# Kernel optimization log

Measured on AMD Instinct MI355X. Metric: run time of the kernel, lower is better.

Reference implementation:

```python
import jax, jax.numpy as jnp
import numpy as np

N, F, H, C, E = 100000, 128, 128, 32, 600000


def setup_inputs() -> dict:
    key = jax.random.key(0)
    ks = jax.random.split(key, 8)
    x = jax.random.normal(ks[0], (N, F), dtype=jnp.float32)
    edge_index = jax.random.randint(ks[1], (2, E), 0, N, dtype=jnp.int64)
    s = 1.0 / np.sqrt(F)
    sh = 1.0 / np.sqrt(H)
    W1l = jax.random.uniform(ks[2], (F, H), jnp.float32, -s, s)
    W1r = jax.random.uniform(ks[3], (F, H), jnp.float32, -s, s)
    b1 = jnp.zeros((H,), jnp.float32)
    W2l = jax.random.uniform(ks[4], (H, C), jnp.float32, -sh, sh)
    W2r = jax.random.uniform(ks[5], (H, C), jnp.float32, -sh, sh)
    b2 = jnp.zeros((C,), jnp.float32)
    return {"x": x, "edge_index": edge_index, "W1l": W1l, "b1": b1,
            "W1r": W1r, "W2l": W2l, "b2": b2, "W2r": W2r}


def reference(x, edge_index, W1l, b1, W1r, W2l, b2, W2r):
    # PyG SAGEConv: out = lin_l(mean_{j in N(i)} x_j) + lin_r(x_i)
    # (lin_l has bias, lin_r does not). Dropout is identity in eval mode.
    src, dst = edge_index[0], edge_index[1]
    n = x.shape[0]
    deg = jax.ops.segment_sum(jnp.ones((src.shape[0],), x.dtype), dst, num_segments=n)
    inv_deg = 1.0 / jnp.maximum(deg, 1.0)  # clamp: isolated nodes get 0 agg

    def sage(h, Wl, bl, Wr):
        agg = jax.ops.segment_sum(h[src], dst, num_segments=n)  # [N, d] gather+scatter
        agg = agg * inv_deg[:, None]
        return agg @ Wl + bl + h @ Wr

    h = jax.nn.relu(sage(x, W1l, b1, W1r))
    return sage(h, W2l, b2, W2r)
```

## Files before the change

### kernel.cpp

```cpp
#include <hip/hip_runtime.h>
#include <hip/hip_bf16.h>


#define FDIM 128
#define CDIM 32
#define SCAN_CHUNK 1024
#define PSTR 136

typedef __attribute__((ext_vector_type(8))) short short8;
typedef __attribute__((ext_vector_type(4))) float f32x4;
typedef unsigned short ushort_t;
typedef unsigned int uint_t;

static __device__ __forceinline__ ushort_t f2bf(float f) {
    uint_t u = __float_as_uint(f);
    u += 0x7fffu + ((u >> 16) & 1u);
    return (ushort_t)(u >> 16);
}
static __device__ __forceinline__ float bf2f_lo(uint_t u) {
    return __uint_as_float(u << 16);
}
static __device__ __forceinline__ float bf2f_hi(uint_t u) {
    return __uint_as_float(u & 0xffff0000u);
}


__global__ __launch_bounds__(256) void prep_kernel(
        const float* __restrict__ x, uint_t* __restrict__ xb4, long long total8,
        const int* __restrict__ dst, int* __restrict__ deg, int E, int n,
        const float* __restrict__ W1l, const float* __restrict__ W1r,
        const float* __restrict__ W2l, const float* __restrict__ W2r,
        ushort_t* __restrict__ w1lt, ushort_t* __restrict__ w1rt,
        ushort_t* __restrict__ w2lt, ushort_t* __restrict__ w2rt,
        int CB, int DB) {
    int b = (int)blockIdx.x;
    if (b < CB) {
        long long i = (long long)b * 256 + threadIdx.x;
        if (i >= total8) return;
        const float4* p = (const float4*)x + i * 2;
        float4 v0 = p[0], v1 = p[1];
        uint4 o;
        o.x = (uint_t)f2bf(v0.x) | ((uint_t)f2bf(v0.y) << 16);
        o.y = (uint_t)f2bf(v0.z) | ((uint_t)f2bf(v0.w) << 16);
        o.z = (uint_t)f2bf(v1.x) | ((uint_t)f2bf(v1.y) << 16);
        o.w = (uint_t)f2bf(v1.z) | ((uint_t)f2bf(v1.w) << 16);
        ((uint4*)xb4)[i] = o;
    } else if (b < CB + DB) {
        int e = (b - CB) * 256 + threadIdx.x;
        if (e < E) {
            int d = dst[e];
            if (d >= 0 && d < n) atomicAdd(&deg[d], 1);
        }
    } else {
        int idx = (b - CB - DB) * 256 + threadIdx.x;
        const float* w; ushort_t* wt; int Nc, local;
        if (idx < 16384)      { w = W1l; wt = w1lt; Nc = 128; local = idx; }
        else if (idx < 32768) { w = W1r; wt = w1rt; Nc = 128; local = idx - 16384; }
        else if (idx < 36864) { w = W2l; wt = w2lt; Nc = 32;  local = idx - 32768; }
        else if (idx < 40960) { w = W2r; wt = w2rt; Nc = 32;  local = idx - 36864; }
        else return;
        int nn = local >> 7, kk = local & 127;
        wt[nn * 128 + kk] = f2bf(w[kk * Nc + nn]);
    }
}


__global__ __launch_bounds__(256) void scan1_kernel(
        const int* __restrict__ deg, int* __restrict__ partials, int n) {
    __shared__ int red[256];
    int t = threadIdx.x;
    int base = blockIdx.x * SCAN_CHUNK + t * 4;
    int s = 0;
    if (base + 3 < n) {
        int4 v = *(const int4*)(deg + base);
        s = v.x + v.y + v.z + v.w;
    } else {
        for (int i = 0; i < 4; i++) if (base + i < n) s += deg[base + i];
    }
    red[t] = s;
    __syncthreads();
#pragma unroll
    for (int off = 128; off > 0; off >>= 1) {
        if (t < off) red[t] += red[t + off];
        __syncthreads();
    }
    if (t == 0) partials[blockIdx.x] = red[0];
}

__global__ __launch_bounds__(256) void scan3_kernel(
        const int* __restrict__ deg, const int* __restrict__ partials,
        int* __restrict__ rowptr, float* __restrict__ inv_deg, int n, int SB) {
    __shared__ int s[256];
    int t = threadIdx.x;
    int pre = (t < SB && t < (int)blockIdx.x) ? partials[t] : 0;
    s[t] = pre;
    __syncthreads();
#pragma unroll
    for (int off = 128; off > 0; off >>= 1) {
        if (t < off) s[t] += s[t + off];
        __syncthreads();
    }
    int blockbase = s[0];
    __syncthreads();

    int base = blockIdx.x * SCAN_CHUNK + t * 4;
    int d0 = 0, d1 = 0, d2 = 0, d3 = 0;
    if (base + 3 < n) {
        int4 v = *(const int4*)(deg + base);
        d0 = v.x; d1 = v.y; d2 = v.z; d3 = v.w;
    } else {
        if (base + 0 < n) d0 = deg[base + 0];
        if (base + 1 < n) d1 = deg[base + 1];
        if (base + 2 < n) d2 = deg[base + 2];
        if (base + 3 < n) d3 = deg[base + 3];
    }
    s[t] = d0 + d1 + d2 + d3;
    __syncthreads();
#pragma unroll
    for (int off = 1; off < 256; off <<= 1) {
        int u = (t >= off) ? s[t - off] : 0;
        __syncthreads();
        s[t] += u;
        __syncthreads();
    }
    int run = blockbase + ((t == 0) ? 0 : s[t - 1]);
    int dd[4] = {d0, d1, d2, d3};
#pragma unroll
    for (int i = 0; i < 4; i++) {
        if (base + i < n) {
            rowptr[base + i]  = run;
            inv_deg[base + i] = 1.0f / (float)(dd[i] > 0 ? dd[i] : 1);
            run += dd[i];
        }
    }
}

__global__ void fill_kernel(const int* __restrict__ src, const int* __restrict__ dst,
                            const int* __restrict__ rowptr, int* __restrict__ cursor,
                            int* __restrict__ nbr, int E, int n) {
    int e = blockIdx.x * 256 + threadIdx.x;
    if (e < E) {
        int s = src[e];
        int d = dst[e];
        if (d >= 0 && d < n) {
            int p = atomicAdd(&cursor[d], 1);
            nbr[rowptr[d] + p] = s;
        }
    }
}


__global__ __launch_bounds__(256) void agg1_kernel(
        const uint_t* __restrict__ xbu ,
        const int* __restrict__ rowptr, const int* __restrict__ deg,
        const int* __restrict__ nbr, const float* __restrict__ inv_deg,
        uint_t* __restrict__ aggbu, int n) {
    int t = threadIdx.x;
    int i = blockIdx.x * 4 + (t >> 6);
    if (i >= n) return;
    int lane = t & 63;
    int g    = lane >> 4;
    int l16  = lane & 15;
    int start = rowptr[i];
    int d     = deg[i];
    float s[8] = {0.f, 0.f, 0.f, 0.f, 0.f, 0.f, 0.f, 0.f};
    int e = g;
    for (; e + 4 < d; e += 8) {
        int j0 = nbr[start + e];
        int j1 = nbr[start + e + 4];
        uint4 u0 = *(const uint4*)(xbu + (size_t)j0 * 64 + l16 * 4);
        uint4 u1 = *(const uint4*)(xbu + (size_t)j1 * 64 + l16 * 4);
        s[0] += bf2f_lo(u0.x) + bf2f_lo(u1.x); s[1] += bf2f_hi(u0.x) + bf2f_hi(u1.x);
        s[2] += bf2f_lo(u0.y) + bf2f_lo(u1.y); s[3] += bf2f_hi(u0.y) + bf2f_hi(u1.y);
        s[4] += bf2f_lo(u0.z) + bf2f_lo(u1.z); s[5] += bf2f_hi(u0.z) + bf2f_hi(u1.z);
        s[6] += bf2f_lo(u0.w) + bf2f_lo(u1.w); s[7] += bf2f_hi(u0.w) + bf2f_hi(u1.w);
    }
    if (e < d) {
        int j = nbr[start + e];
        uint4 u = *(const uint4*)(xbu + (size_t)j * 64 + l16 * 4);
        s[0] += bf2f_lo(u.x); s[1] += bf2f_hi(u.x);
        s[2] += bf2f_lo(u.y); s[3] += bf2f_hi(u.y);
        s[4] += bf2f_lo(u.z); s[5] += bf2f_hi(u.z);
        s[6] += bf2f_lo(u.w); s[7] += bf2f_hi(u.w);
    }
#pragma unroll
    for (int k = 0; k < 8; k++) {
        s[k] += __shfl_xor(s[k], 16, 64);
        s[k] += __shfl_xor(s[k], 32, 64);
    }
    if (g == 0) {
        float inv = inv_deg[i];
        uint4 o;
        o.x = (uint_t)f2bf(s[0] * inv) | ((uint_t)f2bf(s[1] * inv) << 16);
        o.y = (uint_t)f2bf(s[2] * inv) | ((uint_t)f2bf(s[3] * inv) << 16);
        o.z = (uint_t)f2bf(s[4] * inv) | ((uint_t)f2bf(s[5] * inv) << 16);
        o.w = (uint_t)f2bf(s[6] * inv) | ((uint_t)f2bf(s[7] * inv) << 16);
        *(uint4*)(aggbu + (size_t)i * 64 + l16 * 4) = o;
    }
}


__global__ __launch_bounds__(512) void fused12_kernel(
        const ushort_t* __restrict__ xb, const ushort_t* __restrict__ aggb,
        const ushort_t* __restrict__ w1lt, const ushort_t* __restrict__ w1rt,
        const ushort_t* __restrict__ w2lt, const ushort_t* __restrict__ w2rt,
        const float* __restrict__ b1,
        ushort_t* __restrict__ z2b, float* __restrict__ r2, int n) {
    __shared__ ushort_t xs[64 * PSTR];
    __shared__ ushort_t as_[64 * PSTR];
    __shared__ ushort_t ws2[2 * 32 * PSTR];

    const int t    = threadIdx.x;
    const int wave = t >> 6;
    const int lane = t & 63;
    const int quad = lane >> 4;
    const int l16  = lane & 15;
    const int row0 = blockIdx.x * 64;
    const int c1   = wave * 16;

#pragma unroll
    for (int it = 0; it < 2; it++) {
        int c   = t + it * 512;
        int row = c >> 4, col = c & 15;
        int grow = row0 + row; if (grow >= n) grow = n - 1;
        size_t goff = (size_t)grow * FDIM + col * 8;
        short8 vx = *(const short8*)(xb + goff);
        short8 va = *(const short8*)(aggb + goff);
        *(short8*)(xs  + row * PSTR + col * 8) = vx;
        *(short8*)(as_ + row * PSTR + col * 8) = va;
    }
#pragma unroll
    for (int it = 0; it < 2; it++) {
        int c = t + it * 512;
        int m = c >> 9, lo = c & 511;
        int row = lo >> 4, col = lo & 15;
        const ushort_t* sw = m ? w2rt : w2lt;
        *(short8*)(ws2 + (m * 32 + row) * PSTR + col * 8) =
            *(const short8*)(sw + row * 128 + col * 8);
    }

    short8 bl1[4], br1[4];
#pragma unroll
    for (int k = 0; k < 4; k++) {
        size_t woff = (size_t)(c1 + l16) * FDIM + k * 32 + quad * 8;
        bl1[k] = *(const short8*)(w1lt + woff);
        br1[k] = *(const short8*)(w1rt + woff);
    }
    float b1c = b1[c1 + l16];

    __syncthreads();

    f32x4 acc1[4];
#pragma unroll
    for (int r = 0; r < 4; r++) acc1[r] = (f32x4){0.f, 0.f, 0.f, 0.f};

#pragma unroll
    for (int k = 0; k < 4; k++) {
        short8 a1[4], a2[4];
#pragma unroll
        for (int r = 0; r < 4; r++) {
            int lro = (r * 16 + l16) * PSTR + k * 32 + quad * 8;
            a1[r] = *(const short8*)(as_ + lro);
            a2[r] = *(const short8*)(xs  + lro);
        }
#pragma unroll
        for (int r = 0; r < 4; r++) {
            acc1[r] = __builtin_amdgcn_mfma_f32_16x16x32_bf16(a1[r], bl1[k], acc1[r], 0, 0, 0);
            acc1[r] = __builtin_amdgcn_mfma_f32_16x16x32_bf16(a2[r], br1[k], acc1[r], 0, 0, 0);
        }
    }

    __syncthreads();

    ushort_t* hs = xs;
#pragma unroll
    for (int r = 0; r < 4; r++)
#pragma unroll
        for (int reg = 0; reg < 4; reg++) {
            int lrow = r * 16 + quad * 4 + reg;
            float v = acc1[r][reg] + b1c;
            v = v > 0.f ? v : 0.f;
            hs[lrow * PSTR + c1 + l16] = f2bf(v);
        }

    __syncthreads();

    const int rs = (wave >> 1) * 16;
    const int c2 = (wave & 1) * 16;
    f32x4 a2l = (f32x4){0.f, 0.f, 0.f, 0.f};
    f32x4 a2r = (f32x4){0.f, 0.f, 0.f, 0.f};
#pragma unroll
    for (int k = 0; k < 4; k++) {
        short8 ah = *(const short8*)(hs  + (rs + l16) * PSTR + k * 32 + quad * 8);
        short8 wl = *(const short8*)(ws2 + (c2 + l16) * PSTR + k * 32 + quad * 8);
        short8 wr = *(const short8*)(ws2 + (32 + c2 + l16) * PSTR + k * 32 + quad * 8);
        a2l = __builtin_amdgcn_mfma_f32_16x16x32_bf16(ah, wl, a2l, 0, 0, 0);
        a2r = __builtin_amdgcn_mfma_f32_16x16x32_bf16(ah, wr, a2r, 0, 0, 0);
    }
#pragma unroll
    for (int reg = 0; reg < 4; reg++) {
        int grow = row0 + rs + quad * 4 + reg;
        if (grow < n) {
            z2b[(size_t)grow * CDIM + c2 + l16] = f2bf(a2l[reg]);
            r2 [(size_t)grow * CDIM + c2 + l16] = a2r[reg];
        }
    }
}


__global__ __launch_bounds__(256) void combine2_kernel(
        const uint_t* __restrict__ z2bu ,
        const int* __restrict__ rowptr, const int* __restrict__ deg,
        const int* __restrict__ nbr, const float* __restrict__ inv_deg,
        const float* __restrict__ b2, const float* __restrict__ r2,
        float* __restrict__ out, int n) {
    int t = threadIdx.x;
    int i = blockIdx.x * 4 + (t >> 6);
    if (i >= n) return;
    int lane = t & 63;
    int g    = lane >> 4;
    int l16  = lane & 15;
    int start = rowptr[i];
    int d     = deg[i];
    float s0 = 0.f, s1 = 0.f;
    int e = g;
    for (; e + 4 < d; e += 8) {
        int j0 = nbr[start + e];
        int j1 = nbr[start + e + 4];
        uint_t u0 = z2bu[(size_t)j0 * 16 + l16];
        uint_t u1 = z2bu[(size_t)j1 * 16 + l16];
        s0 += bf2f_lo(u0) + bf2f_lo(u1);
        s1 += bf2f_hi(u0) + bf2f_hi(u1);
    }
    if (e < d) {
        int j = nbr[start + e];
        uint_t u = z2bu[(size_t)j * 16 + l16];
        s0 += bf2f_lo(u);
        s1 += bf2f_hi(u);
    }
    s0 += __shfl_xor(s0, 16, 64); s0 += __shfl_xor(s0, 32, 64);
    s1 += __shfl_xor(s1, 16, 64); s1 += __shfl_xor(s1, 32, 64);
    if (g == 0) {
        float inv = inv_deg[i];
        float2 rr = *(const float2*)(r2 + (size_t)i * CDIM + l16 * 2);
        float2 o;
        o.x = s0 * inv + rr.x + b2[l16 * 2];
        o.y = s1 * inv + rr.y + b2[l16 * 2 + 1];
        *(float2*)(out + (size_t)i * CDIM + l16 * 2) = o;
    }
}


extern "C" void kernel_launch(void* const* d_in, const int* in_sizes, int n_in,
                              void* d_out, int out_size, void* d_ws, size_t ws_size,
                              hipStream_t stream) {
    const float* x   = (const float*)d_in[0];
    const int*   ei  = (const int*)d_in[1];
    const float* W1l = (const float*)d_in[2];
    const float* b1  = (const float*)d_in[3];
    const float* W1r = (const float*)d_in[4];
    const float* W2l = (const float*)d_in[5];
    const float* b2  = (const float*)d_in[6];
    const float* W2r = (const float*)d_in[7];

    const int N = in_sizes[0] / FDIM;
    const int E = in_sizes[1] / 2;
    const int* src = ei;
    const int* dst = ei + E;

    char* p = (char*)d_ws;
    int*      deg      = (int*)p;      p += (size_t)N * sizeof(int);
    int*      cursor   = (int*)p;      p += (size_t)N * sizeof(int);
    int*      rowptr   = (int*)p;      p += (size_t)N * sizeof(int);
    float*    inv_deg  = (float*)p;    p += (size_t)N * sizeof(float);
    int*      partials = (int*)p;      p += 256 * sizeof(int);
    ushort_t* w1lt     = (ushort_t*)p; p += FDIM * FDIM * sizeof(ushort_t);
    ushort_t* w1rt     = (ushort_t*)p; p += FDIM * FDIM * sizeof(ushort_t);
    ushort_t* w2lt     = (ushort_t*)p; p += FDIM * CDIM * sizeof(ushort_t);
    ushort_t* w2rt     = (ushort_t*)p; p += FDIM * CDIM * sizeof(ushort_t);
    int*      nbr      = (int*)p;      p += (size_t)((E + 3) / 4 * 4) * sizeof(int);
    ushort_t* xb       = (ushort_t*)p; p += (size_t)N * FDIM * sizeof(ushort_t);
    ushort_t* aggb     = (ushort_t*)p; p += (size_t)N * FDIM * sizeof(ushort_t);
    ushort_t* z2b      = (ushort_t*)p; p += (size_t)N * CDIM * sizeof(ushort_t);
    float*    r2       = (float*)p;    p += (size_t)N * CDIM * sizeof(float);

    const int SB = (N + SCAN_CHUNK - 1) / SCAN_CHUNK;
    const long long total8 = (long long)N * FDIM / 8;
    const int CB = (int)((total8 + 255) / 256);
    const int DB = (E + 255) / 256;
    const int WB = (40960 + 255) / 256;

    hipMemsetAsync(deg, 0, 2 * (size_t)N * sizeof(int), stream);

    prep_kernel <<<CB + DB + WB, 256, 0, stream>>>(x, (uint_t*)xb, total8, dst, deg, E, N,
                                                   W1l, W1r, W2l, W2r,
                                                   w1lt, w1rt, w2lt, w2rt, CB, DB);
    scan1_kernel<<<SB, 256, 0, stream>>>(deg, partials, N);
    scan3_kernel<<<SB, 256, 0, stream>>>(deg, partials, rowptr, inv_deg, N, SB);
    fill_kernel <<<DB, 256, 0, stream>>>(src, dst, rowptr, cursor, nbr, E, N);

    agg1_kernel   <<<(N + 3) / 4, 256, 0, stream>>>((const uint_t*)xb, rowptr, deg, nbr,
                                                    inv_deg, (uint_t*)aggb, N);
    fused12_kernel<<<(N + 63) / 64, 512, 0, stream>>>(xb, aggb, w1lt, w1rt, w2lt, w2rt,
                                                      b1, z2b, r2, N);
    combine2_kernel<<<(N + 3) / 4, 256, 0, stream>>>((const uint_t*)z2b, rowptr, deg, nbr,
                                                     inv_deg, b2, r2, (float*)d_out, N);
}
```

Measured before the change: 255.8 us.

## Fuse layer-1 neighbor aggregation into the fused GEMM kernel via shared memory

Moves the layer-1 mean aggregation into fused12_kernel. Each wave gathers 8 rows' neighbor features and writes the bf16 mean straight into shared memory instead of into a global aggb buffer, which removes a 25.6 MB write and re-read plus one launch. Weight B-fragments are now loaded per k-step rather than held in registers, and launch bounds request higher occupancy. Degree counting is also split out of prep_kernel into its own kernel, so the latency-bound gather now sits inside a 512-thread block that also needs sync and LDS, which may cost occupancy and overlap.

```diff
diff --git a/kernel.cpp b/kernel.cpp
--- a/kernel.cpp
+++ b/kernel.cpp
@@ -25,14 +25,23 @@
 }
 
 
+__global__ void deg_kernel(const int* __restrict__ dst, int* __restrict__ deg,
+                           int E, int n) {
+    int e = blockIdx.x * 256 + threadIdx.x;
+    if (e < E) {
+        int d = dst[e];
+        if (d >= 0 && d < n) atomicAdd(&deg[d], 1);
+    }
+}
+
+
 __global__ __launch_bounds__(256) void prep_kernel(
         const float* __restrict__ x, uint_t* __restrict__ xb4, long long total8,
-        const int* __restrict__ dst, int* __restrict__ deg, int E, int n,
         const float* __restrict__ W1l, const float* __restrict__ W1r,
         const float* __restrict__ W2l, const float* __restrict__ W2r,
         ushort_t* __restrict__ w1lt, ushort_t* __restrict__ w1rt,
         ushort_t* __restrict__ w2lt, ushort_t* __restrict__ w2rt,
-        int CB, int DB) {
+        int CB) {
     int b = (int)blockIdx.x;
     if (b < CB) {
         long long i = (long long)b * 256 + threadIdx.x;
@@ -45,14 +54,8 @@
         o.z = (uint_t)f2bf(v1.x) | ((uint_t)f2bf(v1.y) << 16);
         o.w = (uint_t)f2bf(v1.z) | ((uint_t)f2bf(v1.w) << 16);
         ((uint4*)xb4)[i] = o;
-    } else if (b < CB + DB) {
-        int e = (b - CB) * 256 + threadIdx.x;
-        if (e < E) {
-            int d = dst[e];
-            if (d >= 0 && d < n) atomicAdd(&deg[d], 1);
-        }
     } else {
-        int idx = (b - CB - DB) * 256 + threadIdx.x;
+        int idx = (b - CB) * 256 + threadIdx.x;
         const float* w; ushort_t* wt; int Nc, local;
         if (idx < 16384)      { w = W1l; wt = w1lt; Nc = 128; local = idx; }
         else if (idx < 32768) { w = W1r; wt = w1rt; Nc = 128; local = idx - 16384; }
@@ -150,60 +153,12 @@
 }
 
 
-__global__ __launch_bounds__(256) void agg1_kernel(
-        const uint_t* __restrict__ xbu ,
+__global__ __launch_bounds__(512, 6) void fused12_kernel(
+        const ushort_t* __restrict__ xb, const uint_t* __restrict__ xbu,
+        const ushort_t* __restrict__ w1lt, const ushort_t* __restrict__ w1rt,
+        const ushort_t* __restrict__ w2lt, const ushort_t* __restrict__ w2rt,
         const int* __restrict__ rowptr, const int* __restrict__ deg,
         const int* __restrict__ nbr, const float* __restrict__ inv_deg,
-        uint_t* __restrict__ aggbu, int n) {
-    int t = threadIdx.x;
-    int i = blockIdx.x * 4 + (t >> 6);
-    if (i >= n) return;
-    int lane = t & 63;
-    int g    = lane >> 4;
-    int l16  = lane & 15;
-    int start = rowptr[i];
-    int d     = deg[i];
-    float s[8] = {0.f, 0.f, 0.f, 0.f, 0.f, 0.f, 0.f, 0.f};
-    int e = g;
-    for (; e + 4 < d; e += 8) {
-        int j0 = nbr[start + e];
-        int j1 = nbr[start + e + 4];
-        uint4 u0 = *(const uint4*)(xbu + (size_t)j0 * 64 + l16 * 4);
-        uint4 u1 = *(const uint4*)(xbu + (size_t)j1 * 64 + l16 * 4);
-        s[0] += bf2f_lo(u0.x) + bf2f_lo(u1.x); s[1] += bf2f_hi(u0.x) + bf2f_hi(u1.x);
-        s[2] += bf2f_lo(u0.y) + bf2f_lo(u1.y); s[3] += bf2f_hi(u0.y) + bf2f_hi(u1.y);
-        s[4] += bf2f_lo(u0.z) + bf2f_lo(u1.z); s[5] += bf2f_hi(u0.z) + bf2f_hi(u1.z);
-        s[6] += bf2f_lo(u0.w) + bf2f_lo(u1.w); s[7] += bf2f_hi(u0.w) + bf2f_hi(u1.w);
-    }
-    if (e < d) {
-        int j = nbr[start + e];
-        uint4 u = *(const uint4*)(xbu + (size_t)j * 64 + l16 * 4);
-        s[0] += bf2f_lo(u.x); s[1] += bf2f_hi(u.x);
-        s[2] += bf2f_lo(u.y); s[3] += bf2f_hi(u.y);
-        s[4] += bf2f_lo(u.z); s[5] += bf2f_hi(u.z);
-        s[6] += bf2f_lo(u.w); s[7] += bf2f_hi(u.w);
-    }
-#pragma unroll
-    for (int k = 0; k < 8; k++) {
-        s[k] += __shfl_xor(s[k], 16, 64);
-        s[k] += __shfl_xor(s[k], 32, 64);
-    }
-    if (g == 0) {
-        float inv = inv_deg[i];
-        uint4 o;
-        o.x = (uint_t)f2bf(s[0] * inv) | ((uint_t)f2bf(s[1] * inv) << 16);
-        o.y = (uint_t)f2bf(s[2] * inv) | ((uint_t)f2bf(s[3] * inv) << 16);
-        o.z = (uint_t)f2bf(s[4] * inv) | ((uint_t)f2bf(s[5] * inv) << 16);
-        o.w = (uint_t)f2bf(s[6] * inv) | ((uint_t)f2bf(s[7] * inv) << 16);
-        *(uint4*)(aggbu + (size_t)i * 64 + l16 * 4) = o;
-    }
-}
-
-
-__global__ __launch_bounds__(512) void fused12_kernel(
-        const ushort_t* __restrict__ xb, const ushort_t* __restrict__ aggb,
-        const ushort_t* __restrict__ w1lt, const ushort_t* __restrict__ w1rt,
-        const ushort_t* __restrict__ w2lt, const ushort_t* __restrict__ w2rt,
         const float* __restrict__ b1,
         ushort_t* __restrict__ z2b, float* __restrict__ r2, int n) {
     __shared__ ushort_t xs[64 * PSTR];
@@ -223,11 +178,8 @@
         int c   = t + it * 512;
         int row = c >> 4, col = c & 15;
         int grow = row0 + row; if (grow >= n) grow = n - 1;
-        size_t goff = (size_t)grow * FDIM + col * 8;
-        short8 vx = *(const short8*)(xb + goff);
-        short8 va = *(const short8*)(aggb + goff);
-        *(short8*)(xs  + row * PSTR + col * 8) = vx;
-        *(short8*)(as_ + row * PSTR + col * 8) = va;
+        short8 vx = *(const short8*)(xb + (size_t)grow * FDIM + col * 8);
+        *(short8*)(xs + row * PSTR + col * 8) = vx;
     }
 #pragma unroll
     for (int it = 0; it < 2; it++) {
@@ -239,23 +191,60 @@
             *(const short8*)(sw + row * 128 + col * 8);
     }
 
-    short8 bl1[4], br1[4];
+    for (int q = 0; q < 8; q++) {
+        int lrow = wave * 8 + q;
+        int i = row0 + lrow;
+        if (i >= n) break;
+        int start = rowptr[i];
+        int d     = deg[i];
+        float s[8] = {0.f, 0.f, 0.f, 0.f, 0.f, 0.f, 0.f, 0.f};
+        int e = quad;
+        for (; e + 4 < d; e += 8) {
+            int j0 = nbr[start + e];
+            int j1 = nbr[start + e + 4];
+            uint4 u0 = *(const uint4*)(xbu + (size_t)j0 * 64 + l16 * 4);
+            uint4 u1 = *(const uint4*)(xbu + (size_t)j1 * 64 + l16 * 4);
+            s[0] += bf2f_lo(u0.x) + bf2f_lo(u1.x); s[1] += bf2f_hi(u0.x) + bf2f_hi(u1.x);
+            s[2] += bf2f_lo(u0.y) + bf2f_lo(u1.y); s[3] += bf2f_hi(u0.y) + bf2f_hi(u1.y);
+            s[4] += bf2f_lo(u0.z) + bf2f_lo(u1.z); s[5] += bf2f_hi(u0.z) + bf2f_hi(u1.z);
+            s[6] += bf2f_lo(u0.w) + bf2f_lo(u1.w); s[7] += bf2f_hi(u0.w) + bf2f_hi(u1.w);
+        }
+        if (e < d) {
+            int j = nbr[start + e];
+            uint4 u = *(const uint4*)(xbu + (size_t)j * 64 + l16 * 4);
+            s[0] += bf2f_lo(u.x); s[1] += bf2f_hi(u.x);
+            s[2] += bf2f_lo(u.y); s[3] += bf2f_hi(u.y);
+            s[4] += bf2f_lo(u.z); s[5] += bf2f_hi(u.z);
+            s[6] += bf2f_lo(u.w); s[7] += bf2f_hi(u.w);
+        }
+#pragma unroll
+        for (int k = 0; k < 8; k++) {
+            s[k] += __shfl_xor(s[k], 16, 64);
+            s[k] += __shfl_xor(s[k], 32, 64);
+        }
+        if (quad == 0) {
+            float inv = inv_deg[i];
+            uint4 o;
+            o.x = (uint_t)f2bf(s[0] * inv) | ((uint_t)f2bf(s[1] * inv) << 16);
+            o.y = (uint_t)f2bf(s[2] * inv) | ((uint_t)f2bf(s[3] * inv) << 16);
+            o.z = (uint_t)f2bf(s[4] * inv) | ((uint_t)f2bf(s[5] * inv) << 16);
+            o.w = (uint_t)f2bf(s[6] * inv) | ((uint_t)f2bf(s[7] * inv) << 16);
+            *(uint4*)((uint_t*)(as_ + lrow * PSTR) + l16 * 4) = o;
+        }
+    }
+
+    float b1c = b1[c1 + l16];
+    __syncthreads();
+
+    f32x4 acc1[4];
+#pragma unroll
+    for (int r = 0; r < 4; r++) acc1[r] = (f32x4){0.f, 0.f, 0.f, 0.f};
+
 #pragma unroll
     for (int k = 0; k < 4; k++) {
         size_t woff = (size_t)(c1 + l16) * FDIM + k * 32 + quad * 8;
-        bl1[k] = *(const short8*)(w1lt + woff);
-        br1[k] = *(const short8*)(w1rt + woff);
-    }
-    float b1c = b1[c1 + l16];
-
-    __syncthreads();
-
-    f32x4 acc1[4];
-#pragma unroll
-    for (int r = 0; r < 4; r++) acc1[r] = (f32x4){0.f, 0.f, 0.f, 0.f};
-
-#pragma unroll
-    for (int k = 0; k < 4; k++) {
+        short8 bl1 = *(const short8*)(w1lt + woff);
+        short8 br1 = *(const short8*)(w1rt + woff);
         short8 a1[4], a2[4];
 #pragma unroll
         for (int r = 0; r < 4; r++) {
@@ -265,8 +254,8 @@
         }
 #pragma unroll
         for (int r = 0; r < 4; r++) {
-            acc1[r] = __builtin_amdgcn_mfma_f32_16x16x32_bf16(a1[r], bl1[k], acc1[r], 0, 0, 0);
-            acc1[r] = __builtin_amdgcn_mfma_f32_16x16x32_bf16(a2[r], br1[k], acc1[r], 0, 0, 0);
+            acc1[r] = __builtin_amdgcn_mfma_f32_16x16x32_bf16(a1[r], bl1, acc1[r], 0, 0, 0);
+            acc1[r] = __builtin_amdgcn_mfma_f32_16x16x32_bf16(a2[r], br1, acc1[r], 0, 0, 0);
         }
     }
 
@@ -380,7 +369,6 @@
     ushort_t* w2rt     = (ushort_t*)p; p += FDIM * CDIM * sizeof(ushort_t);
     int*      nbr      = (int*)p;      p += (size_t)((E + 3) / 4 * 4) * sizeof(int);
     ushort_t* xb       = (ushort_t*)p; p += (size_t)N * FDIM * sizeof(ushort_t);
-    ushort_t* aggb     = (ushort_t*)p; p += (size_t)N * FDIM * sizeof(ushort_t);
     ushort_t* z2b      = (ushort_t*)p; p += (size_t)N * CDIM * sizeof(ushort_t);
     float*    r2       = (float*)p;    p += (size_t)N * CDIM * sizeof(float);
 
@@ -392,16 +380,17 @@
 
     hipMemsetAsync(deg, 0, 2 * (size_t)N * sizeof(int), stream);
 
-    prep_kernel <<<CB + DB + WB, 256, 0, stream>>>(x, (uint_t*)xb, total8, dst, deg, E, N,
-                                                   W1l, W1r, W2l, W2r,
-                                                   w1lt, w1rt, w2lt, w2rt, CB, DB);
+    prep_kernel <<<CB + WB, 256, 0, stream>>>(x, (uint_t*)xb, total8,
+                                              W1l, W1r, W2l, W2r,
+                                              w1lt, w1rt, w2lt, w2rt, CB);
+    deg_kernel  <<<DB, 256, 0, stream>>>(dst, deg, E, N);
     scan1_kernel<<<SB, 256, 0, stream>>>(deg, partials, N);
     scan3_kernel<<<SB, 256, 0, stream>>>(deg, partials, rowptr, inv_deg, N, SB);
     fill_kernel <<<DB, 256, 0, stream>>>(src, dst, rowptr, cursor, nbr, E, N);
 
-    agg1_kernel   <<<(N + 3) / 4, 256, 0, stream>>>((const uint_t*)xb, rowptr, deg, nbr,
-                                                    inv_deg, (uint_t*)aggb, N);
-    fused12_kernel<<<(N + 63) / 64, 512, 0, stream>>>(xb, aggb, w1lt, w1rt, w2lt, w2rt,
+    fused12_kernel<<<(N + 63) / 64, 512, 0, stream>>>(xb, (const uint_t*)xb,
+                                                      w1lt, w1rt, w2lt, w2rt,
+                                                      rowptr, deg, nbr, inv_deg,
                                                       b1, z2b, r2, N);
     combine2_kernel<<<(N + 3) / 4, 256, 0, stream>>>((const uint_t*)z2b, rowptr, deg, nbr,
                                                      inv_deg, b2, r2, (float*)d_out, N);
```

Measured after the change: 264.1 us. 3.2% more time.
